# Performance work log

Measured on AMD Instinct MI355X. Metric: run time of the kernel, lower is better.

Reference implementation:

```python
import jax, jax.numpy as jnp
import numpy as np


def conv1x1(x, w, b):
    # x: [B,C,H,W], w: [O,C], b: [O] -> [B,O,H,W]
    return jnp.einsum('bchw,oc->bohw', x, w) + b[None, :, None, None]


def maxpool2x2(x):
    B, C, H, W = x.shape
    return x.reshape(B, C, H // 2, 2, W // 2, 2).max(axis=(3, 5))


def setup_inputs() -> dict:
    key = jax.random.key(0)
    ks = jax.random.split(key, 10)
    C = 256
    x = jax.random.normal(ks[0], (16, C, 64, 64), dtype=jnp.float32)
    s = lambda fan_in: 1.0 / np.sqrt(fan_in)
    w_theta = jax.random.normal(ks[1], (C // 8, C), dtype=jnp.float32) * s(C)
    b_theta = jax.random.normal(ks[2], (C // 8,), dtype=jnp.float32) * 0.01
    w_phi = jax.random.normal(ks[3], (C // 8, C), dtype=jnp.float32) * s(C)
    b_phi = jax.random.normal(ks[4], (C // 8,), dtype=jnp.float32) * 0.01
    w_g = jax.random.normal(ks[5], (C // 2, C), dtype=jnp.float32) * s(C)
    b_g = jax.random.normal(ks[6], (C // 2,), dtype=jnp.float32) * 0.01
    w_attn = jax.random.normal(ks[7], (C, C // 2), dtype=jnp.float32) * s(C // 2)
    b_attn = jax.random.normal(ks[8], (C,), dtype=jnp.float32) * 0.01
    sigma = jnp.full((1,), 0.5, dtype=jnp.float32)
    return {"x": x, "w_theta": w_theta, "b_theta": b_theta,
            "w_phi": w_phi, "b_phi": b_phi, "w_g": w_g, "b_g": b_g,
            "w_attn": w_attn, "b_attn": b_attn, "sigma": sigma}


def reference(x, w_theta, b_theta, w_phi, b_phi, w_g, b_g, w_attn, b_attn, sigma):
    B, C, W, H = x.shape
    N = W * H
    N4 = N // 4
    # Q: [B, N, C/8]
    theta = conv1x1(x, w_theta, b_theta).reshape(B, C // 8, N).transpose(0, 2, 1)
    # K: [B, C/8, N/4] (2x2 maxpool downsample)
    phi = maxpool2x2(conv1x1(x, w_phi, b_phi)).reshape(B, C // 8, N4)
    # attention: [B, N, N/4]
    attn = jax.nn.softmax(jnp.einsum('bnc,bcm->bnm', theta, phi), axis=-1)
    # V: [B, N/4, C/2]
    g = maxpool2x2(conv1x1(x, w_g, b_g)).reshape(B, C // 2, N4).transpose(0, 2, 1)
    attn_g = jnp.einsum('bnm,bmc->bnc', attn, g).transpose(0, 2, 1).reshape(B, C // 2, W, H)
    attn_g = conv1x1(attn_g, w_attn, b_attn)
    return x + sigma[0] * attn_g
```

## Files before the change

### kernel.cpp

```cpp
#include <hip/hip_runtime.h>
#include <math.h>

#define BATCH 16
#define CIN   256
#define NPIX  4096
#define NP4   1024
#define DQK   32
#define DV    128
#define KT    64
#define QW    32
#define QT    128

typedef __attribute__((ext_vector_type(8)))  short short8v;
typedef __attribute__((ext_vector_type(16))) float f32x16;

#define ZERO16 {0.f,0.f,0.f,0.f,0.f,0.f,0.f,0.f,0.f,0.f,0.f,0.f,0.f,0.f,0.f,0.f}

__device__ __forceinline__ unsigned short f2bf(float f) {
    unsigned u = __float_as_uint(f);
    u += 0x7FFFu + ((u >> 16) & 1u);
    return (unsigned short)(u >> 16);
}

__device__ __forceinline__ void gload_lds16(const void* g, void* l) {
    __builtin_amdgcn_global_load_lds(
        (const __attribute__((address_space(1))) unsigned int*)g,
        (__attribute__((address_space(3))) unsigned int*)l, 16, 0, 0);
}

__global__ void wcvt_k(const float* __restrict__ wt, const float* __restrict__ wp,
                       const float* __restrict__ wg, const float* __restrict__ wa,
                       unsigned short* __restrict__ wqkv, unsigned short* __restrict__ wab)
{
    int i = blockIdx.x * 256 + threadIdx.x;
    if (i < 192 * 256) {
        int row = i >> 8, c = i & 255;
        float v = row < 32 ? wt[row * 256 + c]
                : row < 64 ? wp[(row - 32) * 256 + c]
                           : wg[(row - 64) * 256 + c];
        wqkv[i] = f2bf(v);
    } else {
        int j = i - 192 * 256;
        if (j < 256 * DV) wab[j] = f2bf(wa[j]);
    }
}

__global__ __launch_bounds__(256, 2) void conv_qkv_k(
    const float* __restrict__ x, const unsigned short* __restrict__ wqkv,
    const float* __restrict__ b_theta, const float* __restrict__ b_phi,
    const float* __restrict__ b_g, unsigned short* __restrict__ Qg,
    unsigned short* __restrict__ Kg, unsigned short* __restrict__ Vg)
{
    __shared__ __align__(16) union {
        unsigned short xs[2][2][128][8];
        float pool[2][160][32];
    } u;

    const int b    = blockIdx.y;
    const int tile = blockIdx.x;
    const int pixb = tile * 128;
    const int t    = threadIdx.x;
    const int wv   = t >> 6, l = t & 63, h = l >> 5, q31 = l & 31;
    const int sp   = t & 127, skb = t >> 7;

    const float* xb = x + (size_t)b * CIN * NPIX + pixb + sp;

    f32x16 acc[6];
#pragma unroll
    for (int i = 0; i < 6; ++i) acc[i] = ZERO16;

    float xr[8];
#pragma unroll
    for (int j = 0; j < 8; ++j) xr[j] = xb[(size_t)(skb * 8 + j) * NPIX];
    {
        unsigned pk[4];
#pragma unroll
        for (int jj = 0; jj < 4; ++jj)
            pk[jj] = f2bf(xr[2*jj]) | ((unsigned)f2bf(xr[2*jj+1]) << 16);
        *(uint4*)&u.xs[0][skb][sp][0] = *(uint4*)pk;
    }
    __syncthreads();

    for (int ks = 0; ks < 16; ++ks) {
        const int cur = ks & 1;
        if (ks < 15) {
            const float* xn = xb + (size_t)((ks + 1) * 16 + skb * 8) * NPIX;
#pragma unroll
            for (int j = 0; j < 8; ++j) xr[j] = xn[(size_t)j * NPIX];
        }
        short8v bf = *(const short8v*)&u.xs[cur][h][wv * 32 + q31][0];
#pragma unroll
        for (int rb = 0; rb < 6; ++rb) {
            short8v af = *(const short8v*)&wqkv[(size_t)(rb * 32 + q31) * 256 + ks * 16 + h * 8];
            acc[rb] = __builtin_amdgcn_mfma_f32_32x32x16_bf16(af, bf, acc[rb], 0, 0, 0);
        }
        if (ks < 15) {
            unsigned pk[4];
#pragma unroll
            for (int jj = 0; jj < 4; ++jj)
                pk[jj] = f2bf(xr[2*jj]) | ((unsigned)f2bf(xr[2*jj+1]) << 16);
            *(uint4*)&u.xs[cur ^ 1][skb][sp][0] = *(uint4*)pk;
        }
        __syncthreads();
    }

    {
        int pix = pixb + wv * 32 + q31;
        unsigned short* qout = &Qg[((size_t)b * NPIX + pix) * DQK];
#pragma unroll
        for (int m = 0; m < 4; ++m) {
            unsigned pk2[2];
            float v0 = acc[0][m*4+0] + b_theta[4*h + 8*m + 0];
            float v1 = acc[0][m*4+1] + b_theta[4*h + 8*m + 1];
            float v2 = acc[0][m*4+2] + b_theta[4*h + 8*m + 2];
            float v3 = acc[0][m*4+3] + b_theta[4*h + 8*m + 3];
            pk2[0] = f2bf(v0) | ((unsigned)f2bf(v1) << 16);
            pk2[1] = f2bf(v2) | ((unsigned)f2bf(v3) << 16);
            *(uint2*)&qout[8*m + 4*h] = *(uint2*)pk2;
        }
    }

#pragma unroll
    for (int rb = 1; rb < 6; ++rb) {
#pragma unroll
        for (int r = 0; r < 16; ++r) {
            float v  = acc[rb][r];
            float o  = __shfl_xor(v, 1);
            float mx = fmaxf(v, o);
            if ((q31 & 1) == 0) {
                int row = (r & 3) + 8 * (r >> 2) + 4 * h;
                u.pool[wv >> 1][(rb - 1) * 32 + row][(wv & 1) * 16 + (q31 >> 1)] = mx;
            }
        }
    }
    __syncthreads();

    {
        int wx = t & 31;
        int pp = tile * 32 + wx;
#pragma unroll
        for (int i = 0; i < 20; ++i) {
            int ch = (t >> 5) * 20 + i;
            float v = fmaxf(u.pool[0][ch][wx], u.pool[1][ch][wx]);
            if (ch < 32) {
                v += b_phi[ch];
                Kg[(((size_t)b * 4 + (ch >> 3)) * NP4 + pp) * 8 + (ch & 7)] = f2bf(v);
            } else {
                int c = ch - 32;
                v += b_g[c];
                Vg[((size_t)b * 128 + (pp >> 3)) * (DV * 8) + (size_t)c * 8 + (pp & 7)] = f2bf(v);
            }
        }
    }
}

__global__ __launch_bounds__(256, 2) void flash_k(
    const unsigned short* __restrict__ Qg, const unsigned short* __restrict__ Kg,
    const unsigned short* __restrict__ Vg, const unsigned short* __restrict__ wab,
    const float* __restrict__ b_attn, const float* __restrict__ sigma,
    const float* __restrict__ x, float* __restrict__ out)
{
    __shared__ __align__(16) union {
        struct {
            unsigned short ks[4 * KT * 8];
            unsigned short vs[8 * DV * 8];
        } s;
        unsigned short os[4][16 * QW * 8];
    } u;

    const int b   = blockIdx.y;
    const int t   = threadIdx.x;
    const int wv  = t >> 6;
    const int l   = t & 63;
    const int h   = l >> 5;
    const int q31 = l & 31;
    const int p0  = blockIdx.x * QT + wv * QW;

    short8v qf0 = *(const short8v*)&Qg[((size_t)b * NPIX + p0 + q31) * DQK + h * 8];
    short8v qf1 = *(const short8v*)&Qg[((size_t)b * NPIX + p0 + q31) * DQK + 16 + h * 8];

    f32x16 o0 = ZERO16, o1 = ZERO16, o2 = ZERO16, o3 = ZERO16;
    float m = -3.0e38f, lsum = 0.f;

    const size_t kbase = (size_t)b * 4 * NP4 * 8;
    const size_t vbase = (size_t)b * 128 * DV * 8;

    for (int kt = 0; kt < NP4 / KT; ++kt) {
#pragma unroll
        for (int j = 0; j < 5; ++j) {
            int cid = wv * 5 + j;
            if (cid < 4) {
                gload_lds16(&Kg[kbase + ((size_t)cid * NP4 + kt * KT + l) * 8],
                            &u.s.ks[cid * 512]);
            } else {
                int c2 = cid - 4;
                gload_lds16(&Vg[vbase + (size_t)kt * 8192 + c2 * 512 + l * 8],
                            &u.s.vs[c2 * 512]);
            }
        }
        __syncthreads();

        f32x16 s0 = ZERO16, s1 = ZERO16;
        {
            short8v kf;
            kf = *(const short8v*)&u.s.ks[((0 + h) * KT + 0 + q31) * 8];
            s0 = __builtin_amdgcn_mfma_f32_32x32x16_bf16(kf, qf0, s0, 0, 0, 0);
            kf = *(const short8v*)&u.s.ks[((2 + h) * KT + 0 + q31) * 8];
            s0 = __builtin_amdgcn_mfma_f32_32x32x16_bf16(kf, qf1, s0, 0, 0, 0);
            kf = *(const short8v*)&u.s.ks[((0 + h) * KT + 32 + q31) * 8];
            s1 = __builtin_amdgcn_mfma_f32_32x32x16_bf16(kf, qf0, s1, 0, 0, 0);
            kf = *(const short8v*)&u.s.ks[((2 + h) * KT + 32 + q31) * 8];
            s1 = __builtin_amdgcn_mfma_f32_32x32x16_bf16(kf, qf1, s1, 0, 0, 0);
        }

        float mx = s0[0];
#pragma unroll
        for (int r = 1; r < 16; ++r) mx = fmaxf(mx, s0[r]);
#pragma unroll
        for (int r = 0; r < 16; ++r) mx = fmaxf(mx, s1[r]);
        mx = fmaxf(mx, __shfl_xor(mx, 32));

        bool nskip = !__all(mx <= m + 8.0f);
        if (nskip) {
            float mnew = fmaxf(m, mx);
            float scale = __expf(m - mnew);
            m = mnew;
            lsum *= scale;
#pragma unroll
            for (int r = 0; r < 16; ++r) {
                float sc = __shfl(scale, (r & 3) + 8 * (r >> 2) + 4 * h);
                o0[r] *= sc; o1[r] *= sc; o2[r] *= sc; o3[r] *= sc;
            }
        }

        float rs = 0.f;
#pragma unroll
        for (int r = 0; r < 16; ++r) { s0[r] = __expf(s0[r] - m); rs += s0[r]; }
#pragma unroll
        for (int r = 0; r < 16; ++r) { s1[r] = __expf(s1[r] - m); rs += s1[r]; }
        rs += __shfl_xor(rs, 32);
        lsum += rs;

        unsigned ca[8], cb[8], da[8], db[8];
#pragma unroll
        for (int j = 0; j < 8; ++j) {
            asm("v_cvt_pk_bf16_f32 %0, %1, %2" : "=v"(ca[j]) : "v"(s0[2*j]), "v"(s0[2*j+1]));
            asm("v_cvt_pk_bf16_f32 %0, %1, %2" : "=v"(cb[j]) : "v"(s1[2*j]), "v"(s1[2*j+1]));
        }
#pragma unroll
        for (int j = 0; j < 8; ++j) {
            da[j] = (unsigned)__shfl_xor((int)ca[j], 32);
            db[j] = (unsigned)__shfl_xor((int)cb[j], 32);
        }
        union { unsigned uu[4]; short8v v; } pa[4];
#pragma unroll
        for (int ksl = 0; ksl < 2; ++ksl) {
            pa[ksl].uu[0]     = h ? da[4*ksl+2] : ca[4*ksl+0];
            pa[ksl].uu[1]     = h ? da[4*ksl+3] : ca[4*ksl+1];
            pa[ksl].uu[2]     = h ? ca[4*ksl+2] : da[4*ksl+0];
            pa[ksl].uu[3]     = h ? ca[4*ksl+3] : da[4*ksl+1];
            pa[2+ksl].uu[0]   = h ? db[4*ksl+2] : cb[4*ksl+0];
            pa[2+ksl].uu[1]   = h ? db[4*ksl+3] : cb[4*ksl+1];
            pa[2+ksl].uu[2]   = h ? cb[4*ksl+2] : db[4*ksl+0];
            pa[2+ksl].uu[3]   = h ? cb[4*ksl+3] : db[4*ksl+1];
        }

#pragma unroll
        for (int ks16 = 0; ks16 < 4; ++ks16) {
            const unsigned short* vrow = &u.s.vs[((ks16 * 2 + h) * DV) * 8];
            o0 = __builtin_amdgcn_mfma_f32_32x32x16_bf16(pa[ks16].v,
                     *(const short8v*)&vrow[(0  + q31) * 8], o0, 0, 0, 0);
            o1 = __builtin_amdgcn_mfma_f32_32x32x16_bf16(pa[ks16].v,
                     *(const short8v*)&vrow[(32 + q31) * 8], o1, 0, 0, 0);
            o2 = __builtin_amdgcn_mfma_f32_32x32x16_bf16(pa[ks16].v,
                     *(const short8v*)&vrow[(64 + q31) * 8], o2, 0, 0, 0);
            o3 = __builtin_amdgcn_mfma_f32_32x32x16_bf16(pa[ks16].v,
                     *(const short8v*)&vrow[(96 + q31) * 8], o3, 0, 0, 0);
        }
        __syncthreads();
    }

    float rinv = 1.0f / lsum;
    unsigned short* osw = u.os[wv];
#pragma unroll
    for (int r = 0; r < 16; ++r) {
        float rn = __shfl(rinv, (r & 3) + 8 * (r >> 2) + 4 * h);
        int q = (r & 3) + 8 * (r >> 2) + 4 * h;
        osw[((0 * 4 + (q31 >> 3)) * QW + q) * 8 + (l & 7)] = f2bf(o0[r] * rn);
        osw[((1 * 4 + (q31 >> 3)) * QW + q) * 8 + (l & 7)] = f2bf(o1[r] * rn);
        osw[((2 * 4 + (q31 >> 3)) * QW + q) * 8 + (l & 7)] = f2bf(o2[r] * rn);
        osw[((3 * 4 + (q31 >> 3)) * QW + q) * 8 + (l & 7)] = f2bf(o3[r] * rn);
    }

    const float sg = sigma[0];
    for (int cht = 0; cht < 8; ++cht) {
        f32x16 e = ZERO16;
#pragma unroll
        for (int ks16 = 0; ks16 < 8; ++ks16) {
            short8v wf = *(const short8v*)&wab[(size_t)(cht * 32 + q31) * DV + ks16 * 16 + h * 8];
            short8v of = *(const short8v*)&osw[((ks16 * 2 + h) * QW + q31) * 8];
            e = __builtin_amdgcn_mfma_f32_32x32x16_bf16(wf, of, e, 0, 0, 0);
        }
#pragma unroll
        for (int r = 0; r < 16; ++r) {
            int ch = cht * 32 + (r & 3) + 8 * (r >> 2) + 4 * h;
            size_t idx = ((size_t)b * 256 + ch) * NPIX + p0 + q31;
            out[idx] = fmaf(sg, e[r] + b_attn[ch], x[idx]);
        }
    }
}

extern "C" void kernel_launch(void* const* d_in, const int* in_sizes, int n_in,
                              void* d_out, int out_size, void* d_ws, size_t ws_size,
                              hipStream_t stream) {
    const float* x       = (const float*)d_in[0];
    const float* w_theta = (const float*)d_in[1];
    const float* b_theta = (const float*)d_in[2];
    const float* w_phi   = (const float*)d_in[3];
    const float* b_phi   = (const float*)d_in[4];
    const float* w_g     = (const float*)d_in[5];
    const float* b_g     = (const float*)d_in[6];
    const float* w_attn  = (const float*)d_in[7];
    const float* b_attn  = (const float*)d_in[8];
    const float* sigma   = (const float*)d_in[9];
    float* out = (float*)d_out;

    unsigned short* Qg   = (unsigned short*)d_ws;
    unsigned short* Kg   = Qg + (size_t)BATCH * NPIX * DQK;
    unsigned short* Vg   = Kg + (size_t)BATCH * 4 * NP4 * 8;
    unsigned short* wab  = Vg + (size_t)BATCH * 128 * DV * 8;
    unsigned short* wqkv = wab + (size_t)256 * DV;

    wcvt_k    <<<dim3((192 * 256 + 256 * DV + 255) / 256), 256, 0, stream>>>(
        w_theta, w_phi, w_g, w_attn, wqkv, wab);
    conv_qkv_k<<<dim3(NPIX / 128, BATCH), 256, 0, stream>>>(
        x, wqkv, b_theta, b_phi, b_g, Qg, Kg, Vg);
    flash_k   <<<dim3(NPIX / QT, BATCH), 256, 0, stream>>>(
        Qg, Kg, Vg, wab, b_attn, sigma, x, out);
}
```

Before: 104.4 us.

## Double-buffer K/V LDS tiles in flash kernel and restructure QKV x prefetch

The flash attention loop now double-buffers the K and V tiles in LDS. The next tile is issued via global_load_lds before computing on the current one, with one vmcnt(0) wait plus barrier per iteration, so the wait for the load before the first barrier is gone. The QKV projection loop is unrolled by two with two register prefetch sets so global loads for later channel slices overlap the MFMA work. Float-to-bf16 packing uses the hardware v_cvt_pk_bf16_f32 instruction instead of manual rounding. LDS use in flash_k doubles, which may reduce occupancy.

```diff
diff --git a/kernel.cpp b/kernel.cpp
--- a/kernel.cpp
+++ b/kernel.cpp
@@ -22,11 +22,22 @@
     return (unsigned short)(u >> 16);
 }
 
+__device__ __forceinline__ unsigned cvtpk(float a, float b) {
+    unsigned r;
+    asm("v_cvt_pk_bf16_f32 %0, %1, %2" : "=v"(r) : "v"(a), "v"(b));
+    return r;
+}
+
 __device__ __forceinline__ void gload_lds16(const void* g, void* l) {
     __builtin_amdgcn_global_load_lds(
         (const __attribute__((address_space(1))) unsigned int*)g,
         (__attribute__((address_space(3))) unsigned int*)l, 16, 0, 0);
 }
+
+#define VMCNT0_BARRIER() do { \
+    asm volatile("s_waitcnt vmcnt(0)" ::: "memory"); \
+    __syncthreads(); \
+} while (0)
 
 __global__ void wcvt_k(const float* __restrict__ wt, const float* __restrict__ wp,
                        const float* __restrict__ wg, const float* __restrict__ wa,
@@ -69,37 +80,59 @@
 #pragma unroll
     for (int i = 0; i < 6; ++i) acc[i] = ZERO16;
 
-    float xr[8];
-#pragma unroll
-    for (int j = 0; j < 8; ++j) xr[j] = xb[(size_t)(skb * 8 + j) * NPIX];
+    float xa[8], xbr[8];
+#pragma unroll
+    for (int j = 0; j < 8; ++j) xa[j] = xb[(size_t)(skb * 8 + j) * NPIX];
     {
         unsigned pk[4];
 #pragma unroll
-        for (int jj = 0; jj < 4; ++jj)
-            pk[jj] = f2bf(xr[2*jj]) | ((unsigned)f2bf(xr[2*jj+1]) << 16);
+        for (int jj = 0; jj < 4; ++jj) pk[jj] = cvtpk(xa[2*jj], xa[2*jj+1]);
         *(uint4*)&u.xs[0][skb][sp][0] = *(uint4*)pk;
     }
+#pragma unroll
+    for (int j = 0; j < 8; ++j) xbr[j] = xb[(size_t)(16 + skb * 8 + j) * NPIX];
     __syncthreads();
 
-    for (int ks = 0; ks < 16; ++ks) {
-        const int cur = ks & 1;
-        if (ks < 15) {
-            const float* xn = xb + (size_t)((ks + 1) * 16 + skb * 8) * NPIX;
-#pragma unroll
-            for (int j = 0; j < 8; ++j) xr[j] = xn[(size_t)j * NPIX];
-        }
-        short8v bf = *(const short8v*)&u.xs[cur][h][wv * 32 + q31][0];
-#pragma unroll
-        for (int rb = 0; rb < 6; ++rb) {
-            short8v af = *(const short8v*)&wqkv[(size_t)(rb * 32 + q31) * 256 + ks * 16 + h * 8];
-            acc[rb] = __builtin_amdgcn_mfma_f32_32x32x16_bf16(af, bf, acc[rb], 0, 0, 0);
-        }
-        if (ks < 15) {
+    for (int ks = 0; ks < 16; ks += 2) {
+        if (ks < 14) {
+            const float* xn = xb + (size_t)((ks + 2) * 16 + skb * 8) * NPIX;
+#pragma unroll
+            for (int j = 0; j < 8; ++j) xa[j] = xn[(size_t)j * NPIX];
+        }
+        {
+            short8v bf = *(const short8v*)&u.xs[0][h][wv * 32 + q31][0];
+#pragma unroll
+            for (int rb = 0; rb < 6; ++rb) {
+                short8v af = *(const short8v*)&wqkv[(size_t)(rb * 32 + q31) * 256 + ks * 16 + h * 8];
+                acc[rb] = __builtin_amdgcn_mfma_f32_32x32x16_bf16(af, bf, acc[rb], 0, 0, 0);
+            }
+        }
+        {
             unsigned pk[4];
 #pragma unroll
-            for (int jj = 0; jj < 4; ++jj)
-                pk[jj] = f2bf(xr[2*jj]) | ((unsigned)f2bf(xr[2*jj+1]) << 16);
-            *(uint4*)&u.xs[cur ^ 1][skb][sp][0] = *(uint4*)pk;
+            for (int jj = 0; jj < 4; ++jj) pk[jj] = cvtpk(xbr[2*jj], xbr[2*jj+1]);
+            *(uint4*)&u.xs[1][skb][sp][0] = *(uint4*)pk;
+        }
+        __syncthreads();
+
+        if (ks < 14) {
+            const float* xn = xb + (size_t)((ks + 3) * 16 + skb * 8) * NPIX;
+#pragma unroll
+            for (int j = 0; j < 8; ++j) xbr[j] = xn[(size_t)j * NPIX];
+        }
+        {
+            short8v bf = *(const short8v*)&u.xs[1][h][wv * 32 + q31][0];
+#pragma unroll
+            for (int rb = 0; rb < 6; ++rb) {
+                short8v af = *(const short8v*)&wqkv[(size_t)(rb * 32 + q31) * 256 + (ks + 1) * 16 + h * 8];
+                acc[rb] = __builtin_amdgcn_mfma_f32_32x32x16_bf16(af, bf, acc[rb], 0, 0, 0);
+            }
+        }
+        if (ks < 14) {
+            unsigned pk[4];
+#pragma unroll
+            for (int jj = 0; jj < 4; ++jj) pk[jj] = cvtpk(xa[2*jj], xa[2*jj+1]);
+            *(uint4*)&u.xs[0][skb][sp][0] = *(uint4*)pk;
         }
         __syncthreads();
     }
@@ -114,8 +147,8 @@
             float v1 = acc[0][m*4+1] + b_theta[4*h + 8*m + 1];
             float v2 = acc[0][m*4+2] + b_theta[4*h + 8*m + 2];
             float v3 = acc[0][m*4+3] + b_theta[4*h + 8*m + 3];
-            pk2[0] = f2bf(v0) | ((unsigned)f2bf(v1) << 16);
-            pk2[1] = f2bf(v2) | ((unsigned)f2bf(v3) << 16);
+            pk2[0] = cvtpk(v0, v1);
+            pk2[1] = cvtpk(v2, v3);
             *(uint2*)&qout[8*m + 4*h] = *(uint2*)pk2;
         }
     }
@@ -162,8 +195,8 @@
 {
     __shared__ __align__(16) union {
         struct {
-            unsigned short ks[4 * KT * 8];
-            unsigned short vs[8 * DV * 8];
+            unsigned short ks[2][4 * KT * 8];
+            unsigned short vs[2][8 * DV * 8];
         } s;
         unsigned short os[4][16 * QW * 8];
     } u;
@@ -176,40 +209,47 @@
     const int q31 = l & 31;
     const int p0  = blockIdx.x * QT + wv * QW;
 
-    short8v qf0 = *(const short8v*)&Qg[((size_t)b * NPIX + p0 + q31) * DQK + h * 8];
-    short8v qf1 = *(const short8v*)&Qg[((size_t)b * NPIX + p0 + q31) * DQK + 16 + h * 8];
-
-    f32x16 o0 = ZERO16, o1 = ZERO16, o2 = ZERO16, o3 = ZERO16;
-    float m = -3.0e38f, lsum = 0.f;
-
     const size_t kbase = (size_t)b * 4 * NP4 * 8;
     const size_t vbase = (size_t)b * 128 * DV * 8;
 
-    for (int kt = 0; kt < NP4 / KT; ++kt) {
+    auto STAGE = [&](int bu, int kt) {
 #pragma unroll
         for (int j = 0; j < 5; ++j) {
             int cid = wv * 5 + j;
             if (cid < 4) {
                 gload_lds16(&Kg[kbase + ((size_t)cid * NP4 + kt * KT + l) * 8],
-                            &u.s.ks[cid * 512]);
+                            &u.s.ks[bu][cid * 512]);
             } else {
                 int c2 = cid - 4;
                 gload_lds16(&Vg[vbase + (size_t)kt * 8192 + c2 * 512 + l * 8],
-                            &u.s.vs[c2 * 512]);
-            }
-        }
-        __syncthreads();
+                            &u.s.vs[bu][c2 * 512]);
+            }
+        }
+    };
+
+    short8v qf0 = *(const short8v*)&Qg[((size_t)b * NPIX + p0 + q31) * DQK + h * 8];
+    short8v qf1 = *(const short8v*)&Qg[((size_t)b * NPIX + p0 + q31) * DQK + 16 + h * 8];
+
+    f32x16 o0 = ZERO16, o1 = ZERO16, o2 = ZERO16, o3 = ZERO16;
+    float m = -3.0e38f, lsum = 0.f;
+
+    STAGE(0, 0);
+    VMCNT0_BARRIER();
+    int cur = 0;
+
+    for (int kt = 0; kt < NP4 / KT; ++kt) {
+        if (kt < NP4 / KT - 1) STAGE(cur ^ 1, kt + 1);
 
         f32x16 s0 = ZERO16, s1 = ZERO16;
         {
             short8v kf;
-            kf = *(const short8v*)&u.s.ks[((0 + h) * KT + 0 + q31) * 8];
+            kf = *(const short8v*)&u.s.ks[cur][((0 + h) * KT + 0 + q31) * 8];
             s0 = __builtin_amdgcn_mfma_f32_32x32x16_bf16(kf, qf0, s0, 0, 0, 0);
-            kf = *(const short8v*)&u.s.ks[((2 + h) * KT + 0 + q31) * 8];
+            kf = *(const short8v*)&u.s.ks[cur][((2 + h) * KT + 0 + q31) * 8];
             s0 = __builtin_amdgcn_mfma_f32_32x32x16_bf16(kf, qf1, s0, 0, 0, 0);
-            kf = *(const short8v*)&u.s.ks[((0 + h) * KT + 32 + q31) * 8];
+            kf = *(const short8v*)&u.s.ks[cur][((0 + h) * KT + 32 + q31) * 8];
             s1 = __builtin_amdgcn_mfma_f32_32x32x16_bf16(kf, qf0, s1, 0, 0, 0);
-            kf = *(const short8v*)&u.s.ks[((2 + h) * KT + 32 + q31) * 8];
+            kf = *(const short8v*)&u.s.ks[cur][((2 + h) * KT + 32 + q31) * 8];
             s1 = __builtin_amdgcn_mfma_f32_32x32x16_bf16(kf, qf1, s1, 0, 0, 0);
         }
 
@@ -244,8 +284,8 @@
         unsigned ca[8], cb[8], da[8], db[8];
 #pragma unroll
         for (int j = 0; j < 8; ++j) {
-            asm("v_cvt_pk_bf16_f32 %0, %1, %2" : "=v"(ca[j]) : "v"(s0[2*j]), "v"(s0[2*j+1]));
-            asm("v_cvt_pk_bf16_f32 %0, %1, %2" : "=v"(cb[j]) : "v"(s1[2*j]), "v"(s1[2*j+1]));
+            ca[j] = cvtpk(s0[2*j], s0[2*j+1]);
+            cb[j] = cvtpk(s1[2*j], s1[2*j+1]);
         }
 #pragma unroll
         for (int j = 0; j < 8; ++j) {
@@ -267,7 +307,7 @@
 
 #pragma unroll
         for (int ks16 = 0; ks16 < 4; ++ks16) {
-            const unsigned short* vrow = &u.s.vs[((ks16 * 2 + h) * DV) * 8];
+            const unsigned short* vrow = &u.s.vs[cur][((ks16 * 2 + h) * DV) * 8];
             o0 = __builtin_amdgcn_mfma_f32_32x32x16_bf16(pa[ks16].v,
                      *(const short8v*)&vrow[(0  + q31) * 8], o0, 0, 0, 0);
             o1 = __builtin_amdgcn_mfma_f32_32x32x16_bf16(pa[ks16].v,
@@ -277,7 +317,9 @@
             o3 = __builtin_amdgcn_mfma_f32_32x32x16_bf16(pa[ks16].v,
                      *(const short8v*)&vrow[(96 + q31) * 8], o3, 0, 0, 0);
         }
-        __syncthreads();
+
+        VMCNT0_BARRIER();
+        cur ^= 1;
     }
 
     float rinv = 1.0f / lsum;
```

Result: faster. 99.49 us (-4.7%).
